# Performance work log

Measured on AMD Instinct MI355X. Metric: run time of the kernel, lower is better.

Reference implementation:

```python
import jax, jax.numpy as jnp
import numpy as np

NUM_EMBEDDINGS = 1024
EMBEDDING_DIM = 256
COMMITMENT_COST = 0.25


def setup_inputs() -> dict:
    key = jax.random.key(0)
    k1, k2 = jax.random.split(key)
    latents = jax.random.normal(k1, (64, EMBEDDING_DIM, 32, 32), dtype=jnp.float32)
    # embedding init: uniform(-1/K, 1/K)
    scale = 1.0 / NUM_EMBEDDINGS
    embedding = jax.random.uniform(k2, (NUM_EMBEDDINGS, EMBEDDING_DIM),
                                   dtype=jnp.float32, minval=-scale, maxval=scale)
    return {"latents": latents, "embedding": embedding}


def reference(latents, embedding):
    B, C, H, W = latents.shape  # C == EMBEDDING_DIM
    lat_t = jnp.transpose(latents, (0, 2, 3, 1))           # [B,H,W,D]
    flat = lat_t.reshape(-1, C)                             # [N,D]
    distances = (jnp.sum(flat * flat, axis=1, keepdims=True)
                 + jnp.sum(embedding * embedding, axis=1)
                 - 2.0 * jnp.matmul(flat, embedding.T))    # [N,K]
    indices = jnp.argmin(distances, axis=1)                 # [N]
    # gather replaces the one-hot matmul (same math)
    quant_flat = embedding[indices]                         # [N,D]
    quant = quant_flat.reshape(lat_t.shape)                 # [B,H,W,D]
    quant = jnp.transpose(quant, (0, 3, 1, 2))              # [B,C,H,W]
    e_latent_loss = jnp.mean((jax.lax.stop_gradient(quant) - latents) ** 2)
    q_latent_loss = jnp.mean((quant - jax.lax.stop_gradient(latents)) ** 2)
    loss = q_latent_loss + COMMITMENT_COST * e_latent_loss
    # straight-through estimator
    quant_st = latents + jax.lax.stop_gradient(quant - latents)
    return quant_st, loss, indices.reshape(B, H, W)
```

## Files before the change

kernel.cpp:

```cpp
#include <hip/hip_runtime.h>
#include <math.h>


#define DIM 256
#define BSTRIDE 262144
#define OUT_LOSS 16777216
#define OUT_IDX  16777217
#define MARGIN_S 3e-4f

#define RG 8
#define RTILE 32
#define RSTRIDE 260

#define WS_LOSS  0
#define WS_COUNT 8
#define WS_ENORM 64
#define WS_EMBH  8192
#define WS_SEL   532480
#define WS_WL    794624

typedef __attribute__((ext_vector_type(8))) short short8;
typedef __attribute__((ext_vector_type(4))) float f32x4;

__device__ inline unsigned short f2bf(float f) {
  unsigned u = __float_as_uint(f);
  unsigned r = 0x7FFFu + ((u >> 16) & 1u);
  return (unsigned short)((u + r) >> 16);
}
__device__ inline float bf2f(unsigned short h) {
  return __uint_as_float(((unsigned)h) << 16);
}

__global__ void k_init(const float* __restrict__ emb, unsigned short* __restrict__ embHi,
                       float* __restrict__ enormQ, double* __restrict__ lossAcc,
                       int* __restrict__ count) {
  const int t = threadIdx.x;
  if (blockIdx.x == 0 && t == 0) { *lossAcc = 0.0; *count = 0; }
  const int i = (blockIdx.x * 256 + t) * 4;
  float4 v = *(const float4*)(emb + i);
  unsigned r0 = (unsigned)f2bf(v.x) | ((unsigned)f2bf(v.y) << 16);
  unsigned r1 = (unsigned)f2bf(v.z) | ((unsigned)f2bf(v.w) << 16);
  uint2 st; st.x = r0; st.y = r1;
  *(uint2*)(embHi + i) = st;
  if (blockIdx.x < 4) {
    const int k = blockIdx.x * 256 + t;
    const float* e = emb + (size_t)k * DIM;
    float blk[2];
    #pragma unroll
    for (int h = 0; h < 2; ++h) {
      const float* a = e + h * 128;
      float r[8];
      #pragma unroll
      for (int j = 0; j < 8; ++j) r[j] = __fmul_rn(a[j], a[j]);
      for (int ii = 8; ii < 128; ii += 8)
        #pragma unroll
        for (int j = 0; j < 8; ++j) r[j] = __fadd_rn(r[j], __fmul_rn(a[ii+j], a[ii+j]));
      blk[h] = __fadd_rn(__fadd_rn(__fadd_rn(r[0], r[1]), __fadd_rn(r[2], r[3])),
                         __fadd_rn(__fadd_rn(r[4], r[5]), __fadd_rn(r[6], r[7])));
    }
    enormQ[k] = __fadd_rn(blk[0], blk[1]);
  }
}

__launch_bounds__(256, 3)
__global__ void k_score(const float* __restrict__ lat,
                        const unsigned short* __restrict__ embHi,
                        const float* __restrict__ enormQ,
                        int* __restrict__ selIdx, float* __restrict__ out,
                        int* __restrict__ count, int* __restrict__ worklist) {
  __shared__ __align__(16) unsigned short sB[2 * 8192];
  __shared__ float sNorm[1024];

  const int t = threadIdx.x;
  const int w = t >> 6;
  const int L = t & 63;
  const int lane15 = L & 15;
  const int quad = L >> 4;

  const int pix0 = blockIdx.x * 64;
  const int bImg = pix0 >> 10;
  const int hw0 = pix0 & 1023;

  const int nSrc = L & 31;
  const int oSub = L >> 5;

  #pragma unroll
  for (int i = 0; i < 4; ++i) {
    const int o = (w * 4 + i) * 2 + oSub;
    const unsigned short* src = embHi + ((size_t)nSrc * 256 + o * 8);
    unsigned short* dst = sB + (w * 4 + i) * 512;
    __builtin_amdgcn_global_load_lds(
        (const __attribute__((address_space(1))) unsigned int*)src,
        (__attribute__((address_space(3))) unsigned int*)dst, 16, 0, 0);
  }

  for (int i = t; i < 1024; i += 256) sNorm[i] = enormQ[i];

  const int myPixHw = hw0 + w * 16 + lane15;
  const float* latPix = lat + (size_t)bImg * BSTRIDE + myPixHw;
  short8 aHi[8], aLo[8];
  #pragma unroll
  for (int ks = 0; ks < 8; ++ks) {
    #pragma unroll
    for (int j = 0; j < 8; ++j) {
      float f = latPix[(size_t)(ks * 32 + quad * 8 + j) * 1024];
      unsigned short hb = f2bf(f);
      unsigned short lb = f2bf(f - bf2f(hb));
      aHi[ks][j] = (short)hb;
      aLo[ks][j] = (short)lb;
    }
  }

  float b1[4], b2[4];
  int i1[4], i2[4];
  #pragma unroll
  for (int r = 0; r < 4; ++r) { b1[r] = INFINITY; b2[r] = INFINITY; i1[r] = 0x7fffffff; i2[r] = 0x7fffffff; }

  __syncthreads();

  for (int ch = 0; ch < 32; ++ch) {
    const int cur = ch & 1;
    if (ch < 31) {
      #pragma unroll
      for (int i = 0; i < 4; ++i) {
        const int o = (w * 4 + i) * 2 + oSub;
        const unsigned short* src = embHi + ((size_t)((ch + 1) * 32 + nSrc) * 256 + o * 8);
        unsigned short* dst = sB + (1 - cur) * 8192 + (w * 4 + i) * 512;
        __builtin_amdgcn_global_load_lds(
            (const __attribute__((address_space(1))) unsigned int*)src,
            (__attribute__((address_space(3))) unsigned int*)dst, 16, 0, 0);
      }
    }
    const unsigned short* bbuf = sB + cur * 8192;
    f32x4 acc0 = {0.f,0.f,0.f,0.f};
    f32x4 acc1 = {0.f,0.f,0.f,0.f};
    #pragma unroll
    for (int ks = 0; ks < 8; ++ks) {
      const unsigned short* base = bbuf + (size_t)(ks * 128 + quad * 32) * 8;
      short8 bf0 = *(const short8*)(base + lane15 * 8);
      short8 bf1 = *(const short8*)(base + (16 + lane15) * 8);
      acc0 = __builtin_amdgcn_mfma_f32_16x16x32_bf16(aHi[ks], bf0, acc0, 0, 0, 0);
      acc1 = __builtin_amdgcn_mfma_f32_16x16x32_bf16(aHi[ks], bf1, acc1, 0, 0, 0);
      acc0 = __builtin_amdgcn_mfma_f32_16x16x32_bf16(aLo[ks], bf0, acc0, 0, 0, 0);
      acc1 = __builtin_amdgcn_mfma_f32_16x16x32_bf16(aLo[ks], bf1, acc1, 0, 0, 0);
    }
    const int n0 = ch * 32 + lane15;
    const float en0 = sNorm[n0];
    const float en1 = sNorm[n0 + 16];
    #pragma unroll
    for (int r = 0; r < 4; ++r) {
      float s = fmaf(-2.0f, acc0[r], en0);
      if (s < b1[r])      { b2[r] = b1[r]; i2[r] = i1[r]; b1[r] = s; i1[r] = n0; }
      else if (s < b2[r]) { b2[r] = s; i2[r] = n0; }
      float s1 = fmaf(-2.0f, acc1[r], en1);
      if (s1 < b1[r])      { b2[r] = b1[r]; i2[r] = i1[r]; b1[r] = s1; i1[r] = n0 + 16; }
      else if (s1 < b2[r]) { b2[r] = s1; i2[r] = n0 + 16; }
    }
    if (ch < 31) __syncthreads();
  }

  #pragma unroll
  for (int m = 1; m <= 8; m <<= 1) {
    #pragma unroll
    for (int r = 0; r < 4; ++r) {
      float ob1 = __shfl_xor(b1[r], m), ob2 = __shfl_xor(b2[r], m);
      int oi1 = __shfl_xor(i1[r], m), oi2 = __shfl_xor(i2[r], m);
      bool aF = (b1[r] < ob1) || (b1[r] == ob1 && i1[r] < oi1);
      float w1 = aF ? b1[r] : ob1;  int wi1 = aF ? i1[r] : oi1;
      float lf = aF ? ob1 : b1[r];  int lfi = aF ? oi1 : i1[r];
      float ws = aF ? b2[r] : ob2;  int wsi = aF ? i2[r] : oi2;
      bool sF = (ws < lf) || (ws == lf && wsi < lfi);
      b1[r] = w1; i1[r] = wi1;
      b2[r] = sF ? ws : lf; i2[r] = sF ? wsi : lfi;
    }
  }
  if (lane15 == 0) {
    #pragma unroll
    for (int r = 0; r < 4; ++r) {
      const int pix = pix0 + w * 16 + quad * 4 + r;
      if (b2[r] - b1[r] >= MARGIN_S) {
        selIdx[pix] = i1[r];
        out[OUT_IDX + pix] = (float)i1[r];
      } else {
        int pos = atomicAdd(count, 1);
        worklist[pos] = pix;
      }
    }
  }
}

__launch_bounds__(256, 2)
__global__ void k_refine(const float* __restrict__ lat, const float* __restrict__ emb,
                         const float* __restrict__ enormQ,
                         const int* __restrict__ count, const int* __restrict__ worklist,
                         int* __restrict__ selIdx, float* __restrict__ out) {
  __shared__ __align__(16) float sE[RTILE * RSTRIDE];
  __shared__ __align__(16) float sX[RG * RSTRIDE];
  __shared__ float sSx[RG];
  const int t = threadIdx.x;
  const int cnt = *count;
  if (cnt == 0) return;
  const int ngroups = (cnt + RG - 1) / RG;
  const int w = t >> 6, lane = t & 63;
  const int sub = lane >> 5;
  const int kLane = lane & 31;
  const int pixSlot = w * 2 + sub;

  for (int g = blockIdx.x; g < ngroups; g += gridDim.x) {
    {
      const int p = t >> 5, c0 = t & 31;
      int wi = g * RG + p; if (wi >= cnt) wi = cnt - 1;
      const int pix = worklist[wi];
      const float* latB = lat + (size_t)(pix >> 10) * BSTRIDE + (pix & 1023);
      #pragma unroll
      for (int i = 0; i < 8; ++i) {
        int c = c0 + 32 * i;
        sX[p * RSTRIDE + c] = latB[(size_t)c * 1024];
      }
    }
    __syncthreads();
    if (t < RG) {
      const float* a0 = sX + t * RSTRIDE;
      float blk[2];
      #pragma unroll
      for (int h = 0; h < 2; ++h) {
        const float* a = a0 + h * 128;
        float r[8];
        #pragma unroll
        for (int j = 0; j < 8; ++j) r[j] = __fmul_rn(a[j], a[j]);
        for (int i = 8; i < 128; i += 8)
          #pragma unroll
          for (int j = 0; j < 8; ++j) r[j] = __fadd_rn(r[j], __fmul_rn(a[i+j], a[i+j]));
        blk[h] = __fadd_rn(__fadd_rn(__fadd_rn(r[0], r[1]), __fadd_rn(r[2], r[3])),
                           __fadd_rn(__fadd_rn(r[4], r[5]), __fadd_rn(r[6], r[7])));
      }
      sSx[t] = __fadd_rn(blk[0], blk[1]);
    }

    float best = INFINITY; int bi = 0x7fffffff;
    const float* xrow = sX + pixSlot * RSTRIDE;
    for (int tile = 0; tile < 32; ++tile) {
      __syncthreads();
      {
        const int r = t >> 3, q0 = t & 7;
        const float* src = emb + (size_t)(tile * RTILE + r) * 256;
        #pragma unroll
        for (int i = 0; i < 8; ++i) {
          int q = q0 + 8 * i;
          *(float4*)(sE + r * RSTRIDE + q * 4) = *(const float4*)(src + q * 4);
        }
      }
      __syncthreads();
      const float* erow = sE + kLane * RSTRIDE;
      float d = 0.f;
      for (int c = 0; c < 256; c += 4) {
        float4 xv = *(const float4*)(xrow + c);
        float4 ev = *(const float4*)(erow + c);
        d = fmaf(xv.x, ev.x, d); d = fmaf(xv.y, ev.y, d);
        d = fmaf(xv.z, ev.z, d); d = fmaf(xv.w, ev.w, d);
      }
      const int k = tile * RTILE + kLane;
      float dq = __fsub_rn(__fadd_rn(sSx[pixSlot], enormQ[k]), __fmul_rn(2.0f, d));
      if (dq < best) { best = dq; bi = k; }
    }
    for (int off = 16; off > 0; off >>= 1) {
      float ob = __shfl_down(best, off);
      int oi = __shfl_down(bi, off);
      if (ob < best || (ob == best && oi < bi)) { best = ob; bi = oi; }
    }
    if (kLane == 0) {
      const int wi = g * RG + pixSlot;
      if (wi < cnt) {
        const int pix = worklist[wi];
        selIdx[pix] = bi;
        out[OUT_IDX + pix] = (float)bi;
      }
    }
    __syncthreads();
  }
}

__global__ void k_gather(const float* __restrict__ lat, const float* __restrict__ emb,
                         const int* __restrict__ selIdx,
                         float* __restrict__ out, double* __restrict__ lossAcc) {
  __shared__ int sIdx[64];
  const int t = threadIdx.x;
  const int pix0 = blockIdx.x * 64;
  const int b = pix0 >> 10;
  const int hw0 = pix0 & 1023;
  const float* latBase = lat + (size_t)b * BSTRIDE + hw0;

  if (t < 64) sIdx[t] = selIdx[pix0 + t];
  __syncthreads();

  const int cSub = t >> 4;
  const int p4 = (t & 15) * 4;
  const int k0 = sIdx[p4], k1 = sIdx[p4+1], k2 = sIdx[p4+2], k3 = sIdx[p4+3];
  double lsum = 0.0;
  #pragma unroll 4
  for (int i = 0; i < 16; ++i) {
    int c = i * 16 + cSub;
    float4 l = *(const float4*)(latBase + (size_t)c * 1024 + p4);
    float q0 = emb[k0 * DIM + c], q1 = emb[k1 * DIM + c],
          q2 = emb[k2 * DIM + c], q3 = emb[k3 * DIM + c];
    float d0 = q0 - l.x, d1 = q1 - l.y, d2 = q2 - l.z, d3 = q3 - l.w;
    float4 o; o.x = l.x + d0; o.y = l.y + d1; o.z = l.z + d2; o.w = l.w + d3;
    *(float4*)(out + (size_t)b * BSTRIDE + (size_t)c * 1024 + hw0 + p4) = o;
    lsum += (double)d0*d0 + (double)d1*d1 + (double)d2*d2 + (double)d3*d3;
  }
  for (int off = 32; off > 0; off >>= 1) lsum += __shfl_down(lsum, off);
  if ((t & 63) == 0) atomicAdd(lossAcc, lsum);
}

__global__ void k_loss(const double* __restrict__ lossAcc, float* __restrict__ out) {
  double m = *lossAcc * (1.0 / 16777216.0);
  out[OUT_LOSS] = (float)(1.25 * m);
}

extern "C" void kernel_launch(void* const* d_in, const int* in_sizes, int n_in,
                              void* d_out, int out_size, void* d_ws, size_t ws_size,
                              hipStream_t stream) {
  const float* lat = (const float*)d_in[0];
  const float* emb = (const float*)d_in[1];
  float* out = (float*)d_out;
  char* ws = (char*)d_ws;
  double* lossAcc = (double*)(ws + WS_LOSS);
  int* count = (int*)(ws + WS_COUNT);
  float* enormQ = (float*)(ws + WS_ENORM);
  unsigned short* embHi = (unsigned short*)(ws + WS_EMBH);
  int* selIdx = (int*)(ws + WS_SEL);
  int* worklist = (int*)(ws + WS_WL);

  k_init<<<dim3(256), dim3(256), 0, stream>>>(emb, embHi, enormQ, lossAcc, count);
  k_score<<<dim3(1024), dim3(256), 0, stream>>>(lat, embHi, enormQ, selIdx, out, count, worklist);
  k_refine<<<dim3(1024), dim3(256), 0, stream>>>(lat, emb, enormQ, count, worklist, selIdx, out);
  k_gather<<<dim3(1024), dim3(256), 0, stream>>>(lat, emb, selIdx, out, lossAcc);
  k_loss<<<dim3(1), dim3(1), 0, stream>>>(lossAcc, out);
}
```

Measured before the change: 441.1 us.

## Load codebook fragments directly from global into registers, dropping LDS staging

Removes the double-buffered LDS staging of the bf16 codebook and the per-chunk block barriers. Each lane now loads its B fragments straight from global memory into registers, with a two-register-set ping-pong, and processes 16 codes per chunk instead of 32. The register increase is absorbed by lowering the launch-bounds occupancy hint from 3 to 2. The trade is repeated global/L2 traffic from every wave, since there is no sharing through LDS, and lower occupancy, in exchange for no barriers.

Result: slower. 535.5 us (+21.4%).

```diff
diff --git a/kernel.cpp b/kernel.cpp
--- a/kernel.cpp
+++ b/kernel.cpp
@@ -62,13 +62,12 @@
   }
 }
 
-__launch_bounds__(256, 3)
+__launch_bounds__(256, 2)
 __global__ void k_score(const float* __restrict__ lat,
                         const unsigned short* __restrict__ embHi,
                         const float* __restrict__ enormQ,
                         int* __restrict__ selIdx, float* __restrict__ out,
                         int* __restrict__ count, int* __restrict__ worklist) {
-  __shared__ __align__(16) unsigned short sB[2 * 8192];
   __shared__ float sNorm[1024];
 
   const int t = threadIdx.x;
@@ -80,19 +79,6 @@
   const int pix0 = blockIdx.x * 64;
   const int bImg = pix0 >> 10;
   const int hw0 = pix0 & 1023;
-
-  const int nSrc = L & 31;
-  const int oSub = L >> 5;
-
-  #pragma unroll
-  for (int i = 0; i < 4; ++i) {
-    const int o = (w * 4 + i) * 2 + oSub;
-    const unsigned short* src = embHi + ((size_t)nSrc * 256 + o * 8);
-    unsigned short* dst = sB + (w * 4 + i) * 512;
-    __builtin_amdgcn_global_load_lds(
-        (const __attribute__((address_space(1))) unsigned int*)src,
-        (__attribute__((address_space(3))) unsigned int*)dst, 16, 0, 0);
-  }
 
   for (int i = t; i < 1024; i += 256) sNorm[i] = enormQ[i];
 
@@ -116,48 +102,48 @@
   #pragma unroll
   for (int r = 0; r < 4; ++r) { b1[r] = INFINITY; b2[r] = INFINITY; i1[r] = 0x7fffffff; i2[r] = 0x7fffffff; }
 
+  const unsigned short* bBase = embHi + (size_t)lane15 * 256 + quad * 8;
+
+#define SCORE_CHUNK(BREG, CH)                                                  \
+  {                                                                            \
+    f32x4 acc = {0.f, 0.f, 0.f, 0.f};                                          \
+    _Pragma("unroll")                                                          \
+    for (int ks = 0; ks < 8; ++ks) {                                           \
+      acc = __builtin_amdgcn_mfma_f32_16x16x32_bf16(aHi[ks], BREG[ks], acc, 0, 0, 0); \
+      acc = __builtin_amdgcn_mfma_f32_16x16x32_bf16(aLo[ks], BREG[ks], acc, 0, 0, 0); \
+    }                                                                          \
+    const int n = (CH) * 16 + lane15;                                          \
+    const float en = sNorm[n];                                                 \
+    _Pragma("unroll")                                                          \
+    for (int r = 0; r < 4; ++r) {                                              \
+      float s = fmaf(-2.0f, acc[r], en);                                       \
+      if (s < b1[r])      { b2[r] = b1[r]; i2[r] = i1[r]; b1[r] = s; i1[r] = n; } \
+      else if (s < b2[r]) { b2[r] = s; i2[r] = n; }                            \
+    }                                                                          \
+  }
+
+  short8 Ba[8], Bb[8];
+  #pragma unroll
+  for (int ks = 0; ks < 8; ++ks)
+    Ba[ks] = *(const short8*)(bBase + (size_t)ks * 32);
+
   __syncthreads();
 
-  for (int ch = 0; ch < 32; ++ch) {
-    const int cur = ch & 1;
-    if (ch < 31) {
-      #pragma unroll
-      for (int i = 0; i < 4; ++i) {
-        const int o = (w * 4 + i) * 2 + oSub;
-        const unsigned short* src = embHi + ((size_t)((ch + 1) * 32 + nSrc) * 256 + o * 8);
-        unsigned short* dst = sB + (1 - cur) * 8192 + (w * 4 + i) * 512;
-        __builtin_amdgcn_global_load_lds(
-            (const __attribute__((address_space(1))) unsigned int*)src,
-            (__attribute__((address_space(3))) unsigned int*)dst, 16, 0, 0);
-      }
-    }
-    const unsigned short* bbuf = sB + cur * 8192;
-    f32x4 acc0 = {0.f,0.f,0.f,0.f};
-    f32x4 acc1 = {0.f,0.f,0.f,0.f};
-    #pragma unroll
-    for (int ks = 0; ks < 8; ++ks) {
-      const unsigned short* base = bbuf + (size_t)(ks * 128 + quad * 32) * 8;
-      short8 bf0 = *(const short8*)(base + lane15 * 8);
-      short8 bf1 = *(const short8*)(base + (16 + lane15) * 8);
-      acc0 = __builtin_amdgcn_mfma_f32_16x16x32_bf16(aHi[ks], bf0, acc0, 0, 0, 0);
-      acc1 = __builtin_amdgcn_mfma_f32_16x16x32_bf16(aHi[ks], bf1, acc1, 0, 0, 0);
-      acc0 = __builtin_amdgcn_mfma_f32_16x16x32_bf16(aLo[ks], bf0, acc0, 0, 0, 0);
-      acc1 = __builtin_amdgcn_mfma_f32_16x16x32_bf16(aLo[ks], bf1, acc1, 0, 0, 0);
-    }
-    const int n0 = ch * 32 + lane15;
-    const float en0 = sNorm[n0];
-    const float en1 = sNorm[n0 + 16];
-    #pragma unroll
-    for (int r = 0; r < 4; ++r) {
-      float s = fmaf(-2.0f, acc0[r], en0);
-      if (s < b1[r])      { b2[r] = b1[r]; i2[r] = i1[r]; b1[r] = s; i1[r] = n0; }
-      else if (s < b2[r]) { b2[r] = s; i2[r] = n0; }
-      float s1 = fmaf(-2.0f, acc1[r], en1);
-      if (s1 < b1[r])      { b2[r] = b1[r]; i2[r] = i1[r]; b1[r] = s1; i1[r] = n0 + 16; }
-      else if (s1 < b2[r]) { b2[r] = s1; i2[r] = n0 + 16; }
-    }
-    if (ch < 31) __syncthreads();
-  }
+  for (int ch = 0; ch < 64; ch += 2) {
+    {
+      const unsigned short* p = bBase + (size_t)(ch + 1) * 16 * 256;
+      #pragma unroll
+      for (int ks = 0; ks < 8; ++ks) Bb[ks] = *(const short8*)(p + (size_t)ks * 32);
+    }
+    SCORE_CHUNK(Ba, ch)
+    if (ch + 2 < 64) {
+      const unsigned short* p = bBase + (size_t)(ch + 2) * 16 * 256;
+      #pragma unroll
+      for (int ks = 0; ks < 8; ++ks) Ba[ks] = *(const short8*)(p + (size_t)ks * 32);
+    }
+    SCORE_CHUNK(Bb, ch + 1)
+  }
+#undef SCORE_CHUNK
 
   #pragma unroll
   for (int m = 1; m <= 8; m <<= 1) {
```
